# Performance work log

Hardware: AMD Instinct MI355X
Metric: run time of the kernel (lower is better)

## Reference

```python
import jax, jax.numpy as jnp
import numpy as np

B, N, C, H = 4, 2048, 768, 12
D = C // H  # 64
EPS = 1e-12


def setup_inputs() -> dict:
    key = jax.random.key(0)
    ks = jax.random.split(key, 8)
    s = 0.02
    return {
        "x": jax.random.normal(ks[0], (B, N, C), dtype=jnp.float32),
        "Wq": jax.random.normal(ks[1], (C, C), dtype=jnp.float32) * s,
        "bq": jnp.zeros((C,), dtype=jnp.float32),
        "Wkv": jax.random.normal(ks[2], (C, 2 * C), dtype=jnp.float32) * s,
        "bkv": jnp.zeros((2 * C,), dtype=jnp.float32),
        "Wproj": jax.random.normal(ks[3], (C, C), dtype=jnp.float32) * s,
        "bproj": jnp.zeros((C,), dtype=jnp.float32),
        "scale": jnp.full((1, H, 1, 1), D ** -0.5, dtype=jnp.float32),
    }


def _l2norm(t):
    # F.normalize(dim=-1): x / max(||x||_2, eps)
    n = jnp.sqrt(jnp.sum(t * t, axis=-1, keepdims=True))
    return t / jnp.maximum(n, EPS)


def reference(x, Wq, bq, Wkv, bkv, Wproj, bproj, scale):
    b, n, c = x.shape
    q = (x @ Wq + bq).reshape(b, n, H, D).transpose(0, 2, 1, 3)        # [B,H,N,D]
    kv = (x @ Wkv + bkv).reshape(b, n, 2, H, D).transpose(2, 0, 3, 1, 4)
    k, v = kv[0], kv[1]                                                # [B,H,N,D]
    q = _l2norm(q)
    k = _l2norm(k)
    attn = jnp.einsum("bhqd,bhkd->bhqk", q, k) * scale                 # [B,H,N,N]
    attn = jax.nn.softmax(attn, axis=-1)
    out = jnp.einsum("bhqk,bhkd->bhqd", attn, v)                       # [B,H,N,D]
    out = out.transpose(0, 2, 1, 3).reshape(b, n, c)
    return out @ Wproj + bproj
```

## Files before the change

kernel.cpp:

```cpp
#include <hip/hip_runtime.h>
#include <hip/hip_bf16.h>
#include <math.h>


typedef short bf16x8 __attribute__((ext_vector_type(8)));
typedef float f32x4 __attribute__((ext_vector_type(4)));

static __device__ __forceinline__ unsigned short f2bf(float f) {
    unsigned int u = __float_as_uint(f);
    unsigned int r = u + 0x7fff + ((u >> 16) & 1);
    return (unsigned short)(r >> 16);
}
static __device__ __forceinline__ unsigned int pack2(float a, float b) {
    return (unsigned int)f2bf(a) | ((unsigned int)f2bf(b) << 16);
}
static __device__ __forceinline__ unsigned int cvtpk(float a, float b) {
    unsigned int r;
    asm("v_cvt_pk_bf16_f32 %0, %1, %2" : "=v"(r) : "v"(a), "v"(b));
    return r;
}
static __device__ __forceinline__ void gl_lds16(const void* g, void* l) {
    __builtin_amdgcn_global_load_lds(
        (const __attribute__((address_space(1))) unsigned int*)g,
        (__attribute__((address_space(3))) unsigned int*)l, 16, 0, 0);
}

__global__ __launch_bounds__(256) void convx_kernel(
    const float* __restrict__ in, unsigned short* __restrict__ out)
{
    size_t i = ((size_t)blockIdx.x * 256 + threadIdx.x) * 8;
    float4 a = *(const float4*)&in[i];
    float4 b = *(const float4*)&in[i + 4];
    uint4 o = make_uint4(pack2(a.x, a.y), pack2(a.z, a.w), pack2(b.x, b.y), pack2(b.z, b.w));
    *(uint4*)&out[i] = o;
}

__global__ __launch_bounds__(256) void convT_kernel(
    const float* __restrict__ A, int ldA, const float* __restrict__ Bs, int ldB, int split,
    unsigned short* __restrict__ out)
{
    __shared__ char tb[8192];
    const int c0 = blockIdx.x * 64, k0 = blockIdx.y * 64;
    const int t = threadIdx.x;
    const int kl = t >> 2, cq = (t & 3) * 16;
    const float* src; int ld; int cbase;
    if (c0 < split) { src = A;  ld = ldA; cbase = c0; }
    else            { src = Bs; ld = ldB; cbase = c0 - split; }
    #pragma unroll
    for (int jj = 0; jj < 4; ++jj) {
        float4 v = *(const float4*)&src[(size_t)(k0 + kl) * ld + cbase + cq + jj * 4];
        float vv[4] = {v.x, v.y, v.z, v.w};
        #pragma unroll
        for (int je = 0; je < 4; ++je) {
            int c = cq + jj * 4 + je;
            *(unsigned short*)(tb + c * 128 + ((kl * 2) ^ ((c & 7) << 4))) = f2bf(vv[je]);
        }
    }
    __syncthreads();
    const int cl = t >> 2, u2 = (t & 3) * 2;
    uint4 r0 = *(const uint4*)(tb + cl * 128 + ((u2 ^ (cl & 7)) << 4));
    uint4 r1 = *(const uint4*)(tb + cl * 128 + (((u2 + 1) ^ (cl & 7)) << 4));
    size_t ob = (size_t)(c0 + cl) * 768 + k0 + (t & 3) * 16;
    *(uint4*)&out[ob] = r0;
    *(uint4*)&out[ob + 8] = r1;
}

__global__ __launch_bounds__(256) void qkv_gemm_kernel(
    const unsigned short* __restrict__ xb, const unsigned short* __restrict__ WT,
    const float* __restrict__ bq, const float* __restrict__ bkv,
    const float* __restrict__ scale,
    unsigned short* __restrict__ Qb, unsigned short* __restrict__ Kb,
    unsigned short* __restrict__ Vtb)
{
    __shared__ char lds[32768] __attribute__((aligned(16)));

    const int ct = blockIdx.x;
    const int row0 = blockIdx.y * 128;
    const int tid = threadIdx.x;
    const int w = tid >> 6, l = tid & 63;
    const int g = l >> 4, ln = l & 15;
    const int wr = w >> 1, wc = w & 1;
    const int col0 = ct * 128;

    const int srow = (w & 1) * 64 + (l >> 3);
    const int su = ((l & 7) ^ (l >> 3)) * 16;
    const char* s = (w < 2)
        ? (const char*)xb + (size_t)(row0 + srow) * 1536 + su
        : (const char*)WT + (size_t)(col0 + srow) * 1536 + su;
    char* dbase = lds + ((w >= 2) ? 16384 : 0) + (w & 1) * 8192;

    f32x4 acc[4][4];
    #pragma unroll
    for (int m = 0; m < 4; ++m)
        #pragma unroll
        for (int n = 0; n < 4; ++n) acc[m][n] = (f32x4){0.f, 0.f, 0.f, 0.f};

    const int arow = (wr * 64 + ln) * 128;
    const int brow = 16384 + (wc * 64 + ln) * 128;
    const int x0 = ((0 + g) ^ (ln & 7)) * 16;
    const int x1 = ((4 + g) ^ (ln & 7)) * 16;

    for (int ks = 0; ks < 12; ++ks) {
        __syncthreads();
        #pragma unroll
        for (int j = 0; j < 8; ++j)
            gl_lds16(s + (size_t)j * 8 * 1536, dbase + j * 1024);
        s += 128;
        __syncthreads();
        #pragma unroll
        for (int kc = 0; kc < 2; ++kc) {
            const int xo = kc ? x1 : x0;
            bf16x8 af[4], bfr[4];
            #pragma unroll
            for (int m = 0; m < 4; ++m) af[m] = *(const bf16x8*)(lds + arow + m * 2048 + xo);
            #pragma unroll
            for (int n = 0; n < 4; ++n) bfr[n] = *(const bf16x8*)(lds + brow + n * 2048 + xo);
            #pragma unroll
            for (int m = 0; m < 4; ++m)
                #pragma unroll
                for (int n = 0; n < 4; ++n)
                    acc[m][n] = __builtin_amdgcn_mfma_f32_16x16x32_bf16(af[m], bfr[n], acc[m][n], 0, 0, 0);
        }
    }

    const int co = col0 + wc * 64 + ln;
    float bv[4];
    #pragma unroll
    for (int n = 0; n < 4; ++n) {
        int c = co + n * 16;
        bv[n] = (c < 768) ? bq[c] : bkv[c - 768];
    }
    const int region = ct / 6;
    const int h = (ct % 6) * 2 + wc;

    if (region < 2) {
        unsigned short* dst = (region == 0) ? Qb : Kb;
        const float post = (region == 0) ? scale[0] * 1.4426950408889634f : 1.0f;
        #pragma unroll
        for (int m = 0; m < 4; ++m) {
            #pragma unroll
            for (int n = 0; n < 4; ++n)
                #pragma unroll
                for (int r = 0; r < 4; ++r) acc[m][n][r] += bv[n];
            #pragma unroll
            for (int r = 0; r < 4; ++r) {
                float ss = 0.f;
                #pragma unroll
                for (int n = 0; n < 4; ++n) ss += acc[m][n][r] * acc[m][n][r];
                ss += __shfl_xor(ss, 1); ss += __shfl_xor(ss, 2);
                ss += __shfl_xor(ss, 4); ss += __shfl_xor(ss, 8);
                float inv = post / fmaxf(sqrtf(ss), 1e-12f);
                int t = row0 + wr * 64 + m * 16 + g * 4 + r;
                int b = t >> 11, nt = t & 2047;
                size_t base = ((size_t)(b * 12 + h) * 2048 + nt) * 64 + ln;
                #pragma unroll
                for (int n = 0; n < 4; ++n)
                    dst[base + n * 16] = f2bf(acc[m][n][r] * inv);
            }
        }
    } else {
        char* tb = lds + w * 8192;
        __syncthreads();
        #pragma unroll
        for (int m = 0; m < 4; ++m)
            #pragma unroll
            for (int n = 0; n < 4; ++n)
                #pragma unroll
                for (int r = 0; r < 4; ++r) {
                    int d = n * 16 + ln;
                    int tok = m * 16 + g * 4 + r;
                    *(unsigned short*)(tb + d * 128 + ((tok * 2) ^ ((d & 7) << 4))) =
                        f2bf(acc[m][n][r] + bv[n]);
                }
        __syncthreads();
        const int t0 = row0 + wr * 64;
        const int b = t0 >> 11, n0 = t0 & 2047;
        #pragma unroll
        for (int i = 0; i < 8; ++i) {
            int d = i * 8 + (l >> 3);
            uint4 v = *(const uint4*)(tb + d * 128 + (((l & 7) ^ (d & 7)) << 4));
            *(uint4*)&Vtb[((size_t)(b * 12 + h) * 64 + d) * 2048 + n0 + (l & 7) * 8] = v;
        }
    }
}

__global__ __launch_bounds__(256) void attn_kernel(
    const unsigned short* __restrict__ Qg, const unsigned short* __restrict__ Kg,
    const unsigned short* __restrict__ Vtg,
    unsigned short* __restrict__ O)
{
    __shared__ char lds[49152] __attribute__((aligned(16)));

    const int bid = blockIdx.y * 16 + blockIdx.x;
    const int swzb = (bid & 7) * 96 + (bid >> 3);
    const int bh  = swzb >> 4;
    const int q0  = (swzb & 15) * 128;

    const int tid = threadIdx.x;
    const int w   = tid >> 6;
    const int l   = tid & 63;
    const int g   = l >> 4;
    const int ln  = l & 15;
    char* Psw = lds + 32768 + w * 4096;

    const int srow = w * 16 + (l >> 3);
    const int su   = ((l & 7) ^ (l >> 3)) * 16;
    const char* kSp = (const char*)Kg  + ((size_t)bh * 2048 + srow) * 128 + su;
    const char* vSp = (const char*)Vtg + ((size_t)bh * 64   + srow) * 4096 + su;
    char* kD = lds + w * 2048;
    char* vD = lds + 16384 + w * 2048;

    bf16x8 qf[2][2];
    #pragma unroll
    for (int qm = 0; qm < 2; ++qm)
        #pragma unroll
        for (int kc = 0; kc < 2; ++kc) {
            int qrow = q0 + w * 32 + qm * 16 + ln;
            qf[qm][kc] = *(const bf16x8*)&Qg[((size_t)bh * 2048 + qrow) * 64 + kc * 32 + g * 8];
        }

    f32x4 oacc[2][4];
    #pragma unroll
    for (int qm = 0; qm < 2; ++qm)
        #pragma unroll
        for (int dn = 0; dn < 4; ++dn) oacc[qm][dn] = (f32x4){0.f, 0.f, 0.f, 0.f};
    float rs[2] = {0.f, 0.f};

    char* pwb = Psw + ln * 128 + ((g * 8) ^ ((ln & 7) << 4));

    #pragma unroll
    for (int i = 0; i < 2; ++i) {
        gl_lds16(kSp + i * 1024, kD + i * 1024);
        gl_lds16(vSp + (size_t)i * 32768, vD + i * 1024);
    }
    kSp += 8192; vSp += 128;
    __syncthreads();

    int cur = 0;
    for (int kt = 0; kt < 32; ++kt) {
        if (kt < 31) {
            int nb = cur ^ 1;
            #pragma unroll
            for (int i = 0; i < 2; ++i) {
                gl_lds16(kSp + i * 1024, kD + nb * 8192 + i * 1024);
                gl_lds16(vSp + (size_t)i * 32768, vD + nb * 8192 + i * 1024);
            }
            kSp += 8192; vSp += 128;
        }
        const char* Ks  = lds + cur * 8192;
        const char* Vts = lds + 16384 + cur * 8192;

        f32x4 s[2][4];
        __builtin_amdgcn_s_setprio(1);
        #pragma unroll
        for (int kn = 0; kn < 4; ++kn) {
            int krow = kn * 16 + ln;
            int ro = krow * 128, swzk = (krow & 7) << 4;
            bf16x8 kf0 = *(const bf16x8*)(Ks + ro + ((g * 16)      ^ swzk));
            bf16x8 kf1 = *(const bf16x8*)(Ks + ro + ((64 + g * 16) ^ swzk));
            s[0][kn] = (f32x4){0.f, 0.f, 0.f, 0.f};
            s[1][kn] = (f32x4){0.f, 0.f, 0.f, 0.f};
            s[0][kn] = __builtin_amdgcn_mfma_f32_16x16x32_bf16(kf0, qf[0][0], s[0][kn], 0, 0, 0);
            s[0][kn] = __builtin_amdgcn_mfma_f32_16x16x32_bf16(kf1, qf[0][1], s[0][kn], 0, 0, 0);
            s[1][kn] = __builtin_amdgcn_mfma_f32_16x16x32_bf16(kf0, qf[1][0], s[1][kn], 0, 0, 0);
            s[1][kn] = __builtin_amdgcn_mfma_f32_16x16x32_bf16(kf1, qf[1][1], s[1][kn], 0, 0, 0);
        }
        __builtin_amdgcn_s_setprio(0);

        #pragma unroll
        for (int qm = 0; qm < 2; ++qm) {
            char* pw = pwb + qm * 2048;
            #pragma unroll
            for (int kn = 0; kn < 4; ++kn) {
                float e0 = __builtin_amdgcn_exp2f(s[qm][kn][0]);
                float e1 = __builtin_amdgcn_exp2f(s[qm][kn][1]);
                float e2 = __builtin_amdgcn_exp2f(s[qm][kn][2]);
                float e3 = __builtin_amdgcn_exp2f(s[qm][kn][3]);
                rs[qm] += (e0 + e1) + (e2 + e3);
                uint2 wv = make_uint2(cvtpk(e0, e1), cvtpk(e2, e3));
                *(uint2*)((char*)((size_t)pw ^ (size_t)(kn << 5))) = wv;
            }
        }

        __builtin_amdgcn_s_setprio(1);
        #pragma unroll
        for (int kc = 0; kc < 2; ++kc) {
            bf16x8 pf0, pf1;
            {
                int qr = ln;
                pf0 = *(const bf16x8*)(Psw + qr * 128 + ((kc * 64 + g * 16) ^ ((qr & 7) << 4)));
            }
            {
                int qr = 16 + ln;
                pf1 = *(const bf16x8*)(Psw + qr * 128 + ((kc * 64 + g * 16) ^ ((qr & 7) << 4)));
            }
            #pragma unroll
            for (int dn = 0; dn < 4; ++dn) {
                int d = dn * 16 + ln;
                bf16x8 vf = *(const bf16x8*)(Vts + d * 128 + ((kc * 64 + g * 16) ^ ((d & 7) << 4)));
                oacc[0][dn] = __builtin_amdgcn_mfma_f32_16x16x32_bf16(pf0, vf, oacc[0][dn], 0, 0, 0);
                oacc[1][dn] = __builtin_amdgcn_mfma_f32_16x16x32_bf16(pf1, vf, oacc[1][dn], 0, 0, 0);
            }
        }
        __builtin_amdgcn_s_setprio(0);

        __syncthreads();
        cur ^= 1;
    }

    const int b = bh / 12, h = bh % 12;
    #pragma unroll
    for (int qm = 0; qm < 2; ++qm) {
        float v = rs[qm];
        v += __shfl_xor(v, 16); v += __shfl_xor(v, 32);
        #pragma unroll
        for (int r = 0; r < 4; ++r) {
            float denom = __shfl(v, (l & 48) + ((l >> 4) << 2) + r);
            float inv = 1.0f / denom;
            int qrg = q0 + w * 32 + qm * 16 + g * 4 + r;
            size_t base = ((size_t)(b * 2048 + qrg)) * 768 + h * 64;
            #pragma unroll
            for (int dn = 0; dn < 4; ++dn)
                O[base + dn * 16 + ln] = f2bf(oacc[qm][dn][r] * inv);
        }
    }
}

__global__ __launch_bounds__(256) void proj_gemm_kernel(
    const unsigned short* __restrict__ Ob, const unsigned short* __restrict__ WT,
    const float* __restrict__ bp, float* __restrict__ out)
{
    __shared__ char lds[32768] __attribute__((aligned(16)));

    const int row0 = blockIdx.y * 128;
    const int col0 = blockIdx.x * 128;
    const int tid = threadIdx.x;
    const int w = tid >> 6, l = tid & 63;
    const int g = l >> 4, ln = l & 15;
    const int wr = w >> 1, wc = w & 1;

    const int srow = (w & 1) * 64 + (l >> 3);
    const int su = ((l & 7) ^ (l >> 3)) * 16;
    const char* s = (w < 2)
        ? (const char*)Ob + (size_t)(row0 + srow) * 1536 + su
        : (const char*)WT + (size_t)(col0 + srow) * 1536 + su;
    char* dbase = lds + ((w >= 2) ? 16384 : 0) + (w & 1) * 8192;

    f32x4 acc[4][4];
    #pragma unroll
    for (int m = 0; m < 4; ++m)
        #pragma unroll
        for (int n = 0; n < 4; ++n) acc[m][n] = (f32x4){0.f, 0.f, 0.f, 0.f};

    const int arow = (wr * 64 + ln) * 128;
    const int brow = 16384 + (wc * 64 + ln) * 128;
    const int x0 = ((0 + g) ^ (ln & 7)) * 16;
    const int x1 = ((4 + g) ^ (ln & 7)) * 16;

    for (int ks = 0; ks < 12; ++ks) {
        __syncthreads();
        #pragma unroll
        for (int j = 0; j < 8; ++j)
            gl_lds16(s + (size_t)j * 8 * 1536, dbase + j * 1024);
        s += 128;
        __syncthreads();
        #pragma unroll
        for (int kc = 0; kc < 2; ++kc) {
            const int xo = kc ? x1 : x0;
            bf16x8 af[4], bfr[4];
            #pragma unroll
            for (int m = 0; m < 4; ++m) af[m] = *(const bf16x8*)(lds + arow + m * 2048 + xo);
            #pragma unroll
            for (int n = 0; n < 4; ++n) bfr[n] = *(const bf16x8*)(lds + brow + n * 2048 + xo);
            #pragma unroll
            for (int m = 0; m < 4; ++m)
                #pragma unroll
                for (int n = 0; n < 4; ++n)
                    acc[m][n] = __builtin_amdgcn_mfma_f32_16x16x32_bf16(af[m], bfr[n], acc[m][n], 0, 0, 0);
        }
    }

    const int co = col0 + wc * 64 + ln;
    float bv[4];
    #pragma unroll
    for (int n = 0; n < 4; ++n) bv[n] = bp[co + n * 16];
    #pragma unroll
    for (int m = 0; m < 4; ++m)
        #pragma unroll
        for (int r = 0; r < 4; ++r) {
            int t = row0 + wr * 64 + m * 16 + g * 4 + r;
            #pragma unroll
            for (int n = 0; n < 4; ++n)
                out[(size_t)t * 768 + co + n * 16] = acc[m][n][r] + bv[n];
        }
}

extern "C" void kernel_launch(void* const* d_in, const int* in_sizes, int n_in,
                              void* d_out, int out_size, void* d_ws, size_t ws_size,
                              hipStream_t stream) {
    const float* x     = (const float*)d_in[0];
    const float* Wq    = (const float*)d_in[1];
    const float* bq    = (const float*)d_in[2];
    const float* Wkv   = (const float*)d_in[3];
    const float* bkv   = (const float*)d_in[4];
    const float* Wp    = (const float*)d_in[5];
    const float* bp    = (const float*)d_in[6];
    const float* scale = (const float*)d_in[7];
    float* out = (float*)d_out;

    unsigned short* ws = (unsigned short*)d_ws;
    const size_t SZ = (size_t)4 * 12 * 2048 * 64;
    unsigned short* xbw   = ws;
    unsigned short* WqkvT = xbw + SZ;
    unsigned short* WprjT = WqkvT + (size_t)2304 * 768;
    unsigned short* Qw    = WprjT + (size_t)768 * 768;
    unsigned short* Kw    = Qw + SZ;
    unsigned short* Vtw   = Kw + SZ;
    unsigned short* Ow    = Vtw + SZ;

    convx_kernel<<<3072, 256, 0, stream>>>(x, xbw);
    convT_kernel<<<dim3(36, 12), 256, 0, stream>>>(Wq, 768, Wkv, 1536, 768, WqkvT);
    convT_kernel<<<dim3(12, 12), 256, 0, stream>>>(Wp, 768, Wp, 768, 768, WprjT);
    qkv_gemm_kernel<<<dim3(18, 64), 256, 0, stream>>>(xbw, WqkvT, bq, bkv, scale, Qw, Kw, Vtw);
    attn_kernel<<<dim3(16, 48), 256, 0, stream>>>(Qw, Kw, Vtw, Ow);
    proj_gemm_kernel<<<dim3(6, 64), 256, 0, stream>>>(Ow, WprjT, bp, out);
}
```

Before: 161.9 us.

## Split attention work across 8 waves with 16 query rows each

The attention kernel goes from 256 to 512 threads. Each wave now owns 16 query rows instead of 32, which halves per-wave accumulators and S registers so more waves can hide latency. The K/V double-buffered loop is manually unrolled by two with fixed LDS offsets, and each thread issues one async load per tile. The trade-off is that every K/V fragment read from LDS now feeds half as many MFMAs, roughly doubling LDS read traffic per FLOP.

```diff
diff --git a/kernel.cpp b/kernel.cpp
--- a/kernel.cpp
+++ b/kernel.cpp
@@ -184,7 +184,7 @@
     }
 }
 
-__global__ __launch_bounds__(256) void attn_kernel(
+__global__ __launch_bounds__(512, 6) void attn_kernel(
     const unsigned short* __restrict__ Qg, const unsigned short* __restrict__ Kg,
     const unsigned short* __restrict__ Vtg,
     unsigned short* __restrict__ O)
@@ -201,128 +201,107 @@
     const int l   = tid & 63;
     const int g   = l >> 4;
     const int ln  = l & 15;
-    char* Psw = lds + 32768 + w * 4096;
-
-    const int srow = w * 16 + (l >> 3);
+
+    const int srow = w * 8 + (l >> 3);
     const int su   = ((l & 7) ^ (l >> 3)) * 16;
-    const char* kSp = (const char*)Kg  + ((size_t)bh * 2048 + srow) * 128 + su;
-    const char* vSp = (const char*)Vtg + ((size_t)bh * 64   + srow) * 4096 + su;
-    char* kD = lds + w * 2048;
-    char* vD = lds + 16384 + w * 2048;
-
-    bf16x8 qf[2][2];
-    #pragma unroll
-    for (int qm = 0; qm < 2; ++qm)
-        #pragma unroll
-        for (int kc = 0; kc < 2; ++kc) {
-            int qrow = q0 + w * 32 + qm * 16 + ln;
-            qf[qm][kc] = *(const bf16x8*)&Qg[((size_t)bh * 2048 + qrow) * 64 + kc * 32 + g * 8];
-        }
-
-    f32x4 oacc[2][4];
-    #pragma unroll
-    for (int qm = 0; qm < 2; ++qm)
-        #pragma unroll
-        for (int dn = 0; dn < 4; ++dn) oacc[qm][dn] = (f32x4){0.f, 0.f, 0.f, 0.f};
-    float rs[2] = {0.f, 0.f};
-
-    char* pwb = Psw + ln * 128 + ((g * 8) ^ ((ln & 7) << 4));
-
-    #pragma unroll
-    for (int i = 0; i < 2; ++i) {
-        gl_lds16(kSp + i * 1024, kD + i * 1024);
-        gl_lds16(vSp + (size_t)i * 32768, vD + i * 1024);
-    }
-    kSp += 8192; vSp += 128;
+    const char* kS = (const char*)Kg  + ((size_t)bh * 2048 + srow) * 128 + su;
+    const char* vS = (const char*)Vtg + ((size_t)bh * 64   + srow) * 4096 + su;
+    char* kD0 = lds + w * 1024;
+    char* vD0 = lds + 16384 + w * 1024;
+
+    bf16x8 qf0, qf1;
+    {
+        const unsigned short* qp = Qg + ((size_t)bh * 2048 + q0 + w * 16 + ln) * 64 + g * 8;
+        qf0 = *(const bf16x8*)qp;
+        qf1 = *(const bf16x8*)(qp + 32);
+    }
+
+    const int swz = (ln & 7) << 4;
+    const int a_rd   = ln * 128 + ((g * 16) ^ swz);
+    const int a_rd64 = a_rd ^ 64;
+    const int pbase = 32768 + w * 2048;
+    const int pw0 = pbase + ln * 128 + ((g * 8) ^ swz);
+    const int pr0 = pbase + ln * 128 + ((g * 16) ^ swz);
+    const int pr1 = pr0 ^ 64;
+
+    f32x4 oacc[4];
+    #pragma unroll
+    for (int dn = 0; dn < 4; ++dn) oacc[dn] = (f32x4){0.f, 0.f, 0.f, 0.f};
+    float rs = 0.f;
+
+    const f32x4 zero4 = (f32x4){0.f, 0.f, 0.f, 0.f};
+
+    auto compute = [&](const int OFF) {
+        f32x4 s[4];
+        __builtin_amdgcn_s_setprio(1);
+        #pragma unroll
+        for (int kn = 0; kn < 4; ++kn) {
+            bf16x8 kf0 = *(const bf16x8*)(lds + OFF + kn * 2048 + a_rd);
+            bf16x8 kf1 = *(const bf16x8*)(lds + OFF + kn * 2048 + a_rd64);
+            s[kn] = __builtin_amdgcn_mfma_f32_16x16x32_bf16(kf0, qf0, zero4, 0, 0, 0);
+            s[kn] = __builtin_amdgcn_mfma_f32_16x16x32_bf16(kf1, qf1, s[kn], 0, 0, 0);
+        }
+        __builtin_amdgcn_s_setprio(0);
+
+        #pragma unroll
+        for (int kn = 0; kn < 4; ++kn) {
+            float e0 = __builtin_amdgcn_exp2f(s[kn][0]);
+            float e1 = __builtin_amdgcn_exp2f(s[kn][1]);
+            float e2 = __builtin_amdgcn_exp2f(s[kn][2]);
+            float e3 = __builtin_amdgcn_exp2f(s[kn][3]);
+            rs += (e0 + e1) + (e2 + e3);
+            *(uint2*)(lds + (pw0 ^ (kn << 5))) = make_uint2(cvtpk(e0, e1), cvtpk(e2, e3));
+        }
+
+        __builtin_amdgcn_s_setprio(1);
+        {
+            bf16x8 pf = *(const bf16x8*)(lds + pr0);
+            #pragma unroll
+            for (int dn = 0; dn < 4; ++dn) {
+                bf16x8 vf = *(const bf16x8*)(lds + 16384 + OFF + dn * 2048 + a_rd);
+                oacc[dn] = __builtin_amdgcn_mfma_f32_16x16x32_bf16(pf, vf, oacc[dn], 0, 0, 0);
+            }
+        }
+        {
+            bf16x8 pf = *(const bf16x8*)(lds + pr1);
+            #pragma unroll
+            for (int dn = 0; dn < 4; ++dn) {
+                bf16x8 vf = *(const bf16x8*)(lds + 16384 + OFF + dn * 2048 + a_rd64);
+                oacc[dn] = __builtin_amdgcn_mfma_f32_16x16x32_bf16(pf, vf, oacc[dn], 0, 0, 0);
+            }
+        }
+        __builtin_amdgcn_s_setprio(0);
+    };
+
+    gl_lds16(kS, kD0); gl_lds16(vS, vD0);
+    kS += 8192; vS += 128;
     __syncthreads();
 
-    int cur = 0;
-    for (int kt = 0; kt < 32; ++kt) {
-        if (kt < 31) {
-            int nb = cur ^ 1;
-            #pragma unroll
-            for (int i = 0; i < 2; ++i) {
-                gl_lds16(kSp + i * 1024, kD + nb * 8192 + i * 1024);
-                gl_lds16(vSp + (size_t)i * 32768, vD + nb * 8192 + i * 1024);
-            }
-            kSp += 8192; vSp += 128;
-        }
-        const char* Ks  = lds + cur * 8192;
-        const char* Vts = lds + 16384 + cur * 8192;
-
-        f32x4 s[2][4];
-        __builtin_amdgcn_s_setprio(1);
-        #pragma unroll
-        for (int kn = 0; kn < 4; ++kn) {
-            int krow = kn * 16 + ln;
-            int ro = krow * 128, swzk = (krow & 7) << 4;
-            bf16x8 kf0 = *(const bf16x8*)(Ks + ro + ((g * 16)      ^ swzk));
-            bf16x8 kf1 = *(const bf16x8*)(Ks + ro + ((64 + g * 16) ^ swzk));
-            s[0][kn] = (f32x4){0.f, 0.f, 0.f, 0.f};
-            s[1][kn] = (f32x4){0.f, 0.f, 0.f, 0.f};
-            s[0][kn] = __builtin_amdgcn_mfma_f32_16x16x32_bf16(kf0, qf[0][0], s[0][kn], 0, 0, 0);
-            s[0][kn] = __builtin_amdgcn_mfma_f32_16x16x32_bf16(kf1, qf[0][1], s[0][kn], 0, 0, 0);
-            s[1][kn] = __builtin_amdgcn_mfma_f32_16x16x32_bf16(kf0, qf[1][0], s[1][kn], 0, 0, 0);
-            s[1][kn] = __builtin_amdgcn_mfma_f32_16x16x32_bf16(kf1, qf[1][1], s[1][kn], 0, 0, 0);
-        }
-        __builtin_amdgcn_s_setprio(0);
-
-        #pragma unroll
-        for (int qm = 0; qm < 2; ++qm) {
-            char* pw = pwb + qm * 2048;
-            #pragma unroll
-            for (int kn = 0; kn < 4; ++kn) {
-                float e0 = __builtin_amdgcn_exp2f(s[qm][kn][0]);
-                float e1 = __builtin_amdgcn_exp2f(s[qm][kn][1]);
-                float e2 = __builtin_amdgcn_exp2f(s[qm][kn][2]);
-                float e3 = __builtin_amdgcn_exp2f(s[qm][kn][3]);
-                rs[qm] += (e0 + e1) + (e2 + e3);
-                uint2 wv = make_uint2(cvtpk(e0, e1), cvtpk(e2, e3));
-                *(uint2*)((char*)((size_t)pw ^ (size_t)(kn << 5))) = wv;
-            }
-        }
-
-        __builtin_amdgcn_s_setprio(1);
-        #pragma unroll
-        for (int kc = 0; kc < 2; ++kc) {
-            bf16x8 pf0, pf1;
-            {
-                int qr = ln;
-                pf0 = *(const bf16x8*)(Psw + qr * 128 + ((kc * 64 + g * 16) ^ ((qr & 7) << 4)));
-            }
-            {
-                int qr = 16 + ln;
-                pf1 = *(const bf16x8*)(Psw + qr * 128 + ((kc * 64 + g * 16) ^ ((qr & 7) << 4)));
-            }
-            #pragma unroll
-            for (int dn = 0; dn < 4; ++dn) {
-                int d = dn * 16 + ln;
-                bf16x8 vf = *(const bf16x8*)(Vts + d * 128 + ((kc * 64 + g * 16) ^ ((d & 7) << 4)));
-                oacc[0][dn] = __builtin_amdgcn_mfma_f32_16x16x32_bf16(pf0, vf, oacc[0][dn], 0, 0, 0);
-                oacc[1][dn] = __builtin_amdgcn_mfma_f32_16x16x32_bf16(pf1, vf, oacc[1][dn], 0, 0, 0);
-            }
-        }
-        __builtin_amdgcn_s_setprio(0);
-
-        __syncthreads();
-        cur ^= 1;
+    #pragma unroll 1
+    for (int it = 0; it < 16; ++it) {
+        gl_lds16(kS, kD0 + 8192); gl_lds16(vS, vD0 + 8192);
+        kS += 8192; vS += 128;
+        compute(0);
+        __syncthreads();
+        if (it < 15) {
+            gl_lds16(kS, kD0); gl_lds16(vS, vD0);
+            kS += 8192; vS += 128;
+        }
+        compute(8192);
+        __syncthreads();
     }
 
     const int b = bh / 12, h = bh % 12;
-    #pragma unroll
-    for (int qm = 0; qm < 2; ++qm) {
-        float v = rs[qm];
-        v += __shfl_xor(v, 16); v += __shfl_xor(v, 32);
-        #pragma unroll
-        for (int r = 0; r < 4; ++r) {
-            float denom = __shfl(v, (l & 48) + ((l >> 4) << 2) + r);
-            float inv = 1.0f / denom;
-            int qrg = q0 + w * 32 + qm * 16 + g * 4 + r;
-            size_t base = ((size_t)(b * 2048 + qrg)) * 768 + h * 64;
-            #pragma unroll
-            for (int dn = 0; dn < 4; ++dn)
-                O[base + dn * 16 + ln] = f2bf(oacc[qm][dn][r] * inv);
-        }
+    float v = rs;
+    v += __shfl_xor(v, 16); v += __shfl_xor(v, 32);
+    #pragma unroll
+    for (int r = 0; r < 4; ++r) {
+        float inv = 1.0f / __shfl(v, g * 4 + r);
+        int qrg = q0 + w * 16 + g * 4 + r;
+        size_t base = ((size_t)(b * 2048 + qrg)) * 768 + h * 64;
+        #pragma unroll
+        for (int dn = 0; dn < 4; ++dn)
+            O[base + dn * 16 + ln] = f2bf(oacc[dn][r] * inv);
     }
 }
 
@@ -422,6 +401,6 @@
     convT_kernel<<<dim3(36, 12), 256, 0, stream>>>(Wq, 768, Wkv, 1536, 768, WqkvT);
     convT_kernel<<<dim3(12, 12), 256, 0, stream>>>(Wp, 768, Wp, 768, 768, WprjT);
     qkv_gemm_kernel<<<dim3(18, 64), 256, 0, stream>>>(xbw, WqkvT, bq, bkv, scale, Qw, Kw, Vtw);
-    attn_kernel<<<dim3(16, 48), 256, 0, stream>>>(Qw, Kw, Vtw, Ow);
+    attn_kernel<<<dim3(16, 48), 512, 0, stream>>>(Qw, Kw, Vtw, Ow);
     proj_gemm_kernel<<<dim3(6, 64), 256, 0, stream>>>(Ow, WprjT, bp, out);
 }
```

Measured after the change: 144.7 us. -10.6%, faster.
